# Optimization experiments

Measured on AMD Instinct MI355X. Metric: run time of the kernel, lower is better.

The kernel has to match this reference:

```python
import jax, jax.numpy as jnp
import numpy as np

B, NQ, NK = 4, 2048, 2048
D_MODEL, H, DK, DV, M = 512, 8, 64, 64, 40


def setup_inputs() -> dict:
    key = jax.random.key(0)
    ks = jax.random.split(key, 12)
    s = 0.02  # param init scale (stand-in for xavier)
    return {
        "queries": jax.random.normal(ks[0], (B, NQ, D_MODEL), jnp.float32),
        "keys": jax.random.normal(ks[1], (B, NK, D_MODEL), jnp.float32),
        "values": jax.random.normal(ks[2], (B, NK, D_MODEL), jnp.float32),
        "attention_weights": jax.random.uniform(ks[3], (B, H, NQ, NK), jnp.float32),
        "attention_mask": jax.random.randint(ks[4], (B, H, NQ, NK), 0, 2) == 1,
        "Wq": jax.random.normal(ks[5], (D_MODEL, H * DK), jnp.float32) * s,
        "bq": jnp.zeros((H * DK,), jnp.float32),
        "Wk": jax.random.normal(ks[6], (D_MODEL, H * DK), jnp.float32) * s,
        "bk": jnp.zeros((H * DK,), jnp.float32),
        "Wv": jax.random.normal(ks[7], (D_MODEL, H * DV), jnp.float32) * s,
        "bv": jnp.zeros((H * DV,), jnp.float32),
        "Wo": jax.random.normal(ks[8], (H * DV, D_MODEL), jnp.float32) * s,
        "bo": jnp.zeros((D_MODEL,), jnp.float32),
        "m_k": jax.random.normal(ks[9], (1, M, H * DK), jnp.float32) * s,
        "m_v": jax.random.normal(ks[10], (1, M, H * DV), jnp.float32) * s,
    }


def reference(queries, keys, values, attention_weights, attention_mask,
              Wq, bq, Wk, bk, Wv, bv, Wo, bo, m_k, m_v):
    b, nq, _ = queries.shape
    nk = keys.shape[1]
    # learned memory slots, scaled and broadcast over batch
    mk = jnp.sqrt(jnp.float32(DK)) * jnp.broadcast_to(m_k, (b, M, H * DK))
    mv = jnp.sqrt(jnp.float32(M)) * jnp.broadcast_to(m_v, (b, M, H * DV))
    q = (queries @ Wq + bq).reshape(b, nq, H, DK).transpose(0, 2, 1, 3)      # (b,h,nq,dk)
    k = jnp.concatenate([keys @ Wk + bk, mk], axis=1)
    k = k.reshape(b, nk + M, H, DK).transpose(0, 2, 3, 1)                     # (b,h,dk,nk+m)
    v = jnp.concatenate([values @ Wv + bv, mv], axis=1)
    v = v.reshape(b, nk + M, H, DV).transpose(0, 2, 1, 3)                     # (b,h,nk+m,dv)
    att = jnp.matmul(q, k) / jnp.sqrt(jnp.float32(DK))                        # (b,h,nq,nk+m)
    att_x = att[..., :nk] * attention_weights
    att_x = jnp.where(attention_mask, -jnp.inf, att_x)
    att = jnp.concatenate([att_x, att[..., nk:]], axis=-1)
    att = jax.nn.softmax(att, axis=-1)
    out = jnp.matmul(att, v).transpose(0, 2, 1, 3).reshape(b, nq, H * DV)
    return out @ Wo + bo
```

## Files before the change

kernel.cpp:

```cpp
#include <hip/hip_runtime.h>
#include <hip/hip_bf16.h>
#include <cstdint>
#include <cstddef>

typedef __bf16 bf16_t;
typedef __bf16 bf16x8 __attribute__((ext_vector_type(8)));
typedef __bf16 bf16x4 __attribute__((ext_vector_type(4)));
typedef float  f32x4  __attribute__((ext_vector_type(4)));

#define B_    4
#define NQ_   2048
#define NK_   2048
#define H_    8
#define MSL_  40
#define NKP_  2112
#define SCL2  0.18033688011112042f

#define GLOAD_LDS16(GP, LP)                                                        \
    __builtin_amdgcn_global_load_lds(                                              \
        (const __attribute__((address_space(1))) unsigned int*)(GP),               \
        (__attribute__((address_space(3))) unsigned int*)(LP), 16, 0, 0)

__global__ __launch_bounds__(256) void setup_fused(
    const float* __restrict__ Wq, const float* __restrict__ Wk,
    const float* __restrict__ Wv, const float* __restrict__ Wo,
    bf16_t* __restrict__ WqT, bf16_t* __restrict__ WkT,
    bf16_t* __restrict__ WvT, bf16_t* __restrict__ WoT,
    const float* __restrict__ m_k, const float* __restrict__ m_v,
    bf16_t* __restrict__ Kbf, bf16_t* __restrict__ Vt,
    const unsigned int* __restrict__ maskw, int* __restrict__ flag)
{
    __shared__ float t[32][33];
    __shared__ int found;
    const int blk = blockIdx.x;
    const int tid = threadIdx.x;

    if (blk < 1024) {
        const int bz = blk >> 8, by = (blk >> 4) & 15, bx = blk & 15;
        const float* src; bf16_t* dst;
        switch (bz) {
            case 0:  src = Wq; dst = WqT; break;
            case 1:  src = Wk; dst = WkT; break;
            case 2:  src = Wv; dst = WvT; break;
            default: src = Wo; dst = WoT; break;
        }
        const int tx = tid & 31, ty = tid >> 5;
        const int x  = bx * 32 + tx;
        const int y0 = by * 32 + ty;
#pragma unroll
        for (int i = 0; i < 32; i += 8)
            t[ty + i][tx] = src[(size_t)(y0 + i) * 512 + x];
        __syncthreads();
        const int ox  = by * 32 + tx;
        const int oy0 = bx * 32 + ty;
#pragma unroll
        for (int i = 0; i < 32; i += 8)
            dst[(size_t)(oy0 + i) * 512 + ox] = (bf16_t)t[tx][ty + i];
    } else if (blk < 2048) {
        int tt = (blk - 1024) * 256 + tid;
        if (tt < 4 * 64 * 512) {
            int c  = tt & 511;
            int mi = (tt >> 9) & 63;
            int b  = tt >> 15;
            float v = (mi < MSL_) ? 8.0f * m_k[mi * 512 + c] : 0.0f;
            Kbf[((size_t)b * NKP_ + NK_ + mi) * 512 + c] = (bf16_t)v;
        } else {
            int t2 = tt - 4 * 64 * 512;
            int mi = t2 & 63;
            int dv = (t2 >> 6) & 63;
            int h  = (t2 >> 12) & 7;
            int b  = t2 >> 15;
            float v = (mi < MSL_) ? 6.324555320336759f * m_v[mi * 512 + h * 64 + dv] : 0.0f;
            Vt[(((size_t)b * H_ + h) * 64 + dv) * NKP_ + NK_ + mi] = (bf16_t)v;
        }
    } else {
        if (tid == 0) found = 0;
        __syncthreads();
        unsigned int acc = 0;
        for (int i = tid; i < 65536; i += 256)
            acc |= (maskw[i] & 0xFFFFFF00u);
        if (acc) found = 1;
        __syncthreads();
        if (tid == 0) *flag = found;
    }
}

template<bool AF32>
__device__ __forceinline__ void gemm_core(
    bf16_t (*As)[128][72], bf16_t (*Bs)[128][72],
    const void* __restrict__ Av, const bf16_t* __restrict__ BT,
    const float* __restrict__ bias, void* __restrict__ dstv,
    int dstBS, int epi, float scale)
{
    const int tid = threadIdx.x;
    const int w = tid >> 6, l = tid & 63, lg = l >> 4, lr = l & 15;
    const int wr = w >> 1, wc = w & 1;
    const int blockM = blockIdx.x * 128, blockN = blockIdx.y * 128;

    f32x4 acc[4][4];
    const f32x4 zv = {0.f, 0.f, 0.f, 0.f};
#pragma unroll
    for (int i = 0; i < 4; i++)
#pragma unroll
        for (int j = 0; j < 4; j++) acc[i][j] = zv;

    const int ar = tid >> 1;
    const int ac = (tid & 1) * 32;

    float4 ra[8];
    uint4  ra16[4];
    uint4  rb[4];

#define GLOADT(K0) do {                                                           \
    if constexpr (AF32) {                                                         \
        const float* arow_ = (const float*)Av + (size_t)(blockM + ar) * 512 + (K0) + ac; \
        _Pragma("unroll") for (int i_ = 0; i_ < 8; i_++)                          \
            ra[i_] = ((const float4*)arow_)[i_];                                  \
    } else {                                                                      \
        const bf16_t* arow_ = (const bf16_t*)Av + (size_t)(blockM + ar) * 512 + (K0) + ac; \
        _Pragma("unroll") for (int i_ = 0; i_ < 4; i_++)                          \
            ra16[i_] = ((const uint4*)arow_)[i_];                                 \
    }                                                                             \
    const bf16_t* brow_ = BT + (size_t)(blockN + ar) * 512 + (K0) + ac;           \
    _Pragma("unroll") for (int i_ = 0; i_ < 4; i_++)                              \
        rb[i_] = ((const uint4*)brow_)[i_];                                       \
} while (0)

#define LDSWRITE(BUF) do {                                                        \
    if constexpr (AF32) {                                                         \
        _Pragma("unroll") for (int i_ = 0; i_ < 8; i_++) {                        \
            float4 v_ = ra[i_];                                                   \
            bf16x4 pk_ = {(bf16_t)v_.x, (bf16_t)v_.y, (bf16_t)v_.z, (bf16_t)v_.w}; \
            *(bf16x4*)&As[BUF][ar][ac + i_ * 4] = pk_;                            \
        }                                                                         \
    } else {                                                                      \
        _Pragma("unroll") for (int i_ = 0; i_ < 4; i_++)                          \
            *(uint4*)&As[BUF][ar][ac + i_ * 8] = ra16[i_];                        \
    }                                                                             \
    _Pragma("unroll") for (int i_ = 0; i_ < 4; i_++)                              \
        *(uint4*)&Bs[BUF][ar][ac + i_ * 8] = rb[i_];                              \
} while (0)

    GLOADT(0);
    LDSWRITE(0);

    for (int kk = 0; kk < 8; kk++) {
        __syncthreads();
        if (kk < 7) GLOADT((kk + 1) * 64);
        const int cb = kk & 1;
#pragma unroll
        for (int ks = 0; ks < 2; ks++) {
            bf16x8 af[4], bfr[4];
#pragma unroll
            for (int mi = 0; mi < 4; mi++)
                af[mi] = *(const bf16x8*)&As[cb][wr * 64 + mi * 16 + lr][ks * 32 + lg * 8];
#pragma unroll
            for (int ni = 0; ni < 4; ni++)
                bfr[ni] = *(const bf16x8*)&Bs[cb][wc * 64 + ni * 16 + lr][ks * 32 + lg * 8];
#pragma unroll
            for (int mi = 0; mi < 4; mi++)
#pragma unroll
                for (int ni = 0; ni < 4; ni++)
                    acc[mi][ni] = __builtin_amdgcn_mfma_f32_16x16x32_bf16(af[mi], bfr[ni], acc[mi][ni], 0, 0, 0);
        }
        if (kk < 7) LDSWRITE(cb ^ 1);
    }

#undef GLOADT
#undef LDSWRITE

    const int colbase = blockN + wc * 64;
    float bias_v[4];
#pragma unroll
    for (int ni = 0; ni < 4; ni++) bias_v[ni] = bias[colbase + ni * 16 + lr];

#pragma unroll
    for (int mi = 0; mi < 4; mi++) {
        const int r0 = blockM + wr * 64 + mi * 16 + lg * 4;
#pragma unroll
        for (int ni = 0; ni < 4; ni++) {
            const int c = colbase + ni * 16 + lr;
            f32x4 v = acc[mi][ni];
            if (epi == 2) {
                float* dst = (float*)dstv;
#pragma unroll
                for (int j = 0; j < 4; j++)
                    dst[(size_t)(r0 + j) * 512 + c] = (v[j] + bias_v[ni]) * scale;
            } else if (epi == 0) {
                bf16_t* dst = (bf16_t*)dstv;
#pragma unroll
                for (int j = 0; j < 4; j++) {
                    int rr = r0 + j;
                    int bb = rr >> 11, nn = rr & 2047;
                    dst[((size_t)bb * dstBS + nn) * 512 + c] = (bf16_t)((v[j] + bias_v[ni]) * scale);
                }
            } else {
                bf16_t* dst = (bf16_t*)dstv;
                int bb = r0 >> 11, n0 = r0 & 2047;
                int hh = c >> 6, dv = c & 63;
                bf16x4 pk;
#pragma unroll
                for (int j = 0; j < 4; j++) pk[j] = (bf16_t)((v[j] + bias_v[ni]) * scale);
                *(bf16x4*)(dst + (((size_t)bb * H_ + hh) * 64 + dv) * NKP_ + n0) = pk;
            }
        }
    }
}

__global__ __launch_bounds__(256) void gemm_qkv(
    const float* __restrict__ q, const float* __restrict__ k, const float* __restrict__ v,
    const bf16_t* __restrict__ WqT, const bf16_t* __restrict__ WkT, const bf16_t* __restrict__ WvT,
    const float* __restrict__ bq, const float* __restrict__ bk, const float* __restrict__ bv,
    bf16_t* __restrict__ Qbf, bf16_t* __restrict__ Kbf, bf16_t* __restrict__ Vt)
{
    __shared__ bf16_t As[2][128][72];
    __shared__ bf16_t Bs[2][128][72];
    const void* Av; const bf16_t* BT; const float* bias; void* dst;
    int dstBS, epi; float scale = 1.0f;
    switch (blockIdx.z) {
        case 0:  Av = q; BT = WqT; bias = bq; dst = Qbf; dstBS = 2048; epi = 0; scale = SCL2; break;
        case 1:  Av = k; BT = WkT; bias = bk; dst = Kbf; dstBS = NKP_; epi = 0; break;
        default: Av = v; BT = WvT; bias = bv; dst = Vt;  dstBS = 0;    epi = 1; break;
    }
    gemm_core<true>(As, Bs, Av, BT, bias, dst, dstBS, epi, scale);
}

__global__ __launch_bounds__(256) void gemm_fin(
    const bf16_t* __restrict__ Obuf, const bf16_t* __restrict__ WoT,
    const float* __restrict__ bo, float* __restrict__ out)
{
    __shared__ bf16_t As[2][128][72];
    __shared__ bf16_t Bs[2][128][72];
    gemm_core<false>(As, Bs, Obuf, WoT, bo, out, 0, 2, 1.0f);
}

template<bool BYTEM>
__global__ __launch_bounds__(512) void attn_fused(
    const bf16_t* __restrict__ Qbf, const bf16_t* __restrict__ Kbf,
    const bf16_t* __restrict__ Vt, const float* __restrict__ attw,
    const void* __restrict__ maskv, const int* __restrict__ mflag,
    bf16_t* __restrict__ Obuf)
{
    if ((*mflag != 0) != BYTEM) return;

    __shared__ bf16_t Ks[4][64][64];
    __shared__ bf16_t Vs[4][64][64];
    __shared__ bf16_t Pl[8][1024];

    const int tid = threadIdx.x;
    const int wv = tid >> 6, l = tid & 63, lg = l >> 4, lr = l & 15;
    const int qt = blockIdx.x, h = blockIdx.y, b = blockIdx.z;
    const int q0w = qt * 128 + wv * 16;
    bf16_t* Pw = &Pl[wv][0];

    const size_t bh = (size_t)(b * H_ + h);
    const float* wbase = attw + bh * (size_t)NQ_ * NK_;
    const unsigned char* mb8 = (const unsigned char*)maskv + bh * (size_t)NQ_ * NK_;
    const int* mb32 = (const int*)maskv + bh * (size_t)NQ_ * NK_;
    const char* kbase8 = (const char*)(Kbf + (size_t)b * NKP_ * 512 + h * 64);
    const char* vbase8 = (const char*)(Vt + bh * 64 * (size_t)NKP_);

    bf16x8 qf0 = *(const bf16x8*)&Qbf[((size_t)b * NQ_ + q0w + lr) * 512 + h * 64 + lg * 8];
    bf16x8 qf1 = *(const bf16x8*)&Qbf[((size_t)b * NQ_ + q0w + lr) * 512 + h * 64 + 32 + lg * 8];

    const f32x4 zv = {0.f, 0.f, 0.f, 0.f};
    f32x4 oacc[4];
#pragma unroll
    for (int i = 0; i < 4; i++) oacc[i] = zv;
    float lsum = 0.f;
    f32x4 sA[4];

    f32x4 wA[4], wB[4];
    unsigned mA[4], mB[4];
    unsigned miA[16], miB[16];

    const int srow = l >> 3;
    const int scsw = ((l & 7) ^ (srow & 7)) * 16;

#define STAGE(BUF, KCB) do {                                                      \
    const int r_ = wv * 8 + srow;                                                 \
    GLOAD_LDS16(kbase8 + (size_t)((KCB) + r_) * 1024 + scsw,                      \
                (char*)&Ks[BUF][0][0] + wv * 1024);                               \
    GLOAD_LDS16(vbase8 + (size_t)r_ * 4224 + (size_t)(KCB) * 2 + scsw,            \
                (char*)&Vs[BUF][0][0] + wv * 1024);                               \
} while (0)

#define PREFETCH(KT, WB_, MB_, MIB_) do {                                         \
    const float* wp_ = wbase + (size_t)(q0w + lr) * NK_ + (KT) * 64 + lg * 4;     \
    _Pragma("unroll") for (int n_ = 0; n_ < 4; n_++)                              \
        WB_[n_] = *(const f32x4*)(wp_ + n_ * 16);                                 \
    if constexpr (BYTEM) {                                                        \
        const unsigned char* mp_ = mb8 + (size_t)(q0w + lr) * NK_ + (KT) * 64 + lg * 4; \
        _Pragma("unroll") for (int n_ = 0; n_ < 4; n_++)                          \
            MB_[n_] = *(const unsigned*)(mp_ + n_ * 16);                          \
    } else {                                                                      \
        const int* mp_ = mb32 + (size_t)(q0w + lr) * NK_ + (KT) * 64 + lg * 4;    \
        _Pragma("unroll") for (int n_ = 0; n_ < 4; n_++) {                        \
            uint4 t_ = *(const uint4*)(mp_ + n_ * 16);                            \
            MIB_[n_ * 4 + 0] = t_.x; MIB_[n_ * 4 + 1] = t_.y;                     \
            MIB_[n_ * 4 + 2] = t_.z; MIB_[n_ * 4 + 3] = t_.w; }                   \
    }                                                                             \
} while (0)

#define QKT_LDS(BC) do {                                                          \
    const int sw_ = (lg ^ (lr & 7)) * 8;                                          \
    _Pragma("unroll") for (int n_ = 0; n_ < 4; n_++) {                            \
        const int kr_ = n_ * 16 + lr;                                             \
        f32x4 a_ = zv;                                                            \
        a_ = __builtin_amdgcn_mfma_f32_16x16x32_bf16(*(const bf16x8*)&Ks[BC][kr_][sw_], qf0, a_, 0, 0, 0); \
        a_ = __builtin_amdgcn_mfma_f32_16x16x32_bf16(*(const bf16x8*)&Ks[BC][kr_][sw_ ^ 32], qf1, a_, 0, 0, 0); \
        sA[n_] = a_;                                                              \
    }                                                                             \
} while (0)

#define APPLY(WB_, MB_, MIB_) do {                                                \
    _Pragma("unroll") for (int n_ = 0; n_ < 4; n_++)                              \
    _Pragma("unroll") for (int j_ = 0; j_ < 4; j_++) {                            \
        bool mk_;                                                                 \
        if constexpr (BYTEM) mk_ = ((MB_[n_] >> (8 * j_)) & 0xffu) != 0;          \
        else                 mk_ = (MIB_[n_ * 4 + j_] != 0);                      \
        sA[n_][j_] = mk_ ? -1e30f : sA[n_][j_] * WB_[n_][j_];                     \
    }                                                                             \
} while (0)

#define SMPV(BC) do {                                                             \
    _Pragma("unroll") for (int n_ = 0; n_ < 4; n_++)                              \
    _Pragma("unroll") for (int j_ = 0; j_ < 4; j_++) {                            \
        float p_ = exp2f(sA[n_][j_]);                                             \
        sA[n_][j_] = p_; lsum += p_;                                              \
    }                                                                             \
    _Pragma("unroll") for (int n_ = 0; n_ < 4; n_++) {                            \
        int c_ = n_ * 2 + (lg >> 1);                                              \
        int qp_ = (lr + 4 * c_) & 15;                                             \
        bf16x4 pk_ = {(bf16_t)sA[n_][0], (bf16_t)sA[n_][1],                       \
                      (bf16_t)sA[n_][2], (bf16_t)sA[n_][3]};                      \
        *(bf16x4*)&Pw[c_ * 128 + qp_ * 8 + (lg & 1) * 4] = pk_;                   \
    }                                                                             \
    bf16x8 pf0_ = *(const bf16x8*)&Pw[lg * 128 + ((lr + 4 * lg) & 15) * 8];       \
    bf16x8 pf1_ = *(const bf16x8*)&Pw[(4 + lg) * 128 + ((lr + 4 * (4 + lg)) & 15) * 8]; \
    const int vsw_ = (lg ^ (lr & 7)) * 8;                                         \
    _Pragma("unroll") for (int n2_ = 0; n2_ < 4; n2_++) {                         \
        const int vr_ = n2_ * 16 + lr;                                            \
        oacc[n2_] = __builtin_amdgcn_mfma_f32_16x16x32_bf16(*(const bf16x8*)&Vs[BC][vr_][vsw_], pf0_, oacc[n2_], 0, 0, 0); \
        oacc[n2_] = __builtin_amdgcn_mfma_f32_16x16x32_bf16(*(const bf16x8*)&Vs[BC][vr_][vsw_ ^ 32], pf1_, oacc[n2_], 0, 0, 0); \
    }                                                                             \
} while (0)

#define SUBB(T, BC, W_, M_, MI_) do {                                            \
    QKT_LDS(BC);                                                                  \
    APPLY(W_, M_, MI_);                                                           \
    if ((T) < 30) PREFETCH((T) + 2, W_, M_, MI_);                                 \
    SMPV(BC);                                                                     \
} while (0)

#define PERIOD(T, B0, B1, S0, S1) do {                                            \
    if ((T) + 2 < 32) STAGE(S0, ((T) + 2) * 64);                                  \
    if ((T) + 3 < 32) STAGE(S1, ((T) + 3) * 64);                                  \
    SUBB((T),     B0, wA, mA, miA);                                               \
    SUBB((T) + 1, B1, wB, mB, miB);                                               \
    __syncthreads();                                                              \
} while (0)

    STAGE(0, 2048);
    STAGE(1, 0);
    STAGE(2, 64);
    PREFETCH(0, wA, mA, miA);
    __syncthreads();

    {
        QKT_LDS(0);
#pragma unroll
        for (int n_ = 0; n_ < 4; n_++)
#pragma unroll
            for (int j_ = 0; j_ < 4; j_++) {
                int kloc = n_ * 16 + lg * 4 + j_;
                sA[n_][j_] = (kloc >= MSL_) ? -1e30f : sA[n_][j_];
            }
        PREFETCH(1, wB, mB, miB);
        SMPV(0);
        __syncthreads();
    }

    for (int t = 0; t < 28; t += 4) {
        PERIOD(t,     1, 2, 3, 0);
        PERIOD(t + 2, 3, 0, 1, 2);
    }
    PERIOD(28, 1, 2, 3, 0);
    SUBB(30, 3, wA, mA, miA);
    SUBB(31, 0, wB, mB, miB);

    float ts = lsum;
    ts += __shfl_xor(ts, 16);
    ts += __shfl_xor(ts, 32);
    float invl = 1.0f / ts;
#pragma unroll
    for (int n2 = 0; n2 < 4; n2++) {
        bf16x4 ov = {(bf16_t)(oacc[n2][0] * invl), (bf16_t)(oacc[n2][1] * invl),
                     (bf16_t)(oacc[n2][2] * invl), (bf16_t)(oacc[n2][3] * invl)};
        *(bf16x4*)&Obuf[((size_t)b * NQ_ + q0w + lr) * 512 + h * 64 + n2 * 16 + lg * 4] = ov;
    }

#undef STAGE
#undef PREFETCH
#undef QKT_LDS
#undef APPLY
#undef SMPV
#undef SUBB
#undef PERIOD
}

extern "C" void kernel_launch(void* const* d_in, const int* in_sizes, int n_in,
                              void* d_out, int out_size, void* d_ws, size_t ws_size,
                              hipStream_t stream)
{
    const float* queries = (const float*)d_in[0];
    const float* keys    = (const float*)d_in[1];
    const float* values  = (const float*)d_in[2];
    const float* attw    = (const float*)d_in[3];
    const void*  maskv   = d_in[4];
    const float* Wq = (const float*)d_in[5];
    const float* bq = (const float*)d_in[6];
    const float* Wk = (const float*)d_in[7];
    const float* bk = (const float*)d_in[8];
    const float* Wv = (const float*)d_in[9];
    const float* bv = (const float*)d_in[10];
    const float* Wo = (const float*)d_in[11];
    const float* bo = (const float*)d_in[12];
    const float* m_k = (const float*)d_in[13];
    const float* m_v = (const float*)d_in[14];

    char* ws = (char*)d_ws;
    bf16_t* WqT  = (bf16_t*)(ws + 0);
    bf16_t* WkT  = (bf16_t*)(ws + 524288);
    bf16_t* WvT  = (bf16_t*)(ws + 1048576);
    bf16_t* WoT  = (bf16_t*)(ws + 1572864);
    bf16_t* Qbf  = (bf16_t*)(ws + 2097152);
    bf16_t* Kbf  = (bf16_t*)(ws + 10485760);
    bf16_t* Vt   = (bf16_t*)(ws + 19136512);
    bf16_t* Obuf = (bf16_t*)(ws + 27787264);
    int*    mflag = (int*)(ws + 36175872);

    setup_fused<<<2049, 256, 0, stream>>>(
        Wq, Wk, Wv, Wo, WqT, WkT, WvT, WoT,
        m_k, m_v, Kbf, Vt, (const unsigned int*)maskv, mflag);

    gemm_qkv<<<dim3(64, 4, 3), 256, 0, stream>>>(
        queries, keys, values, WqT, WkT, WvT, bq, bk, bv, Qbf, Kbf, Vt);

    attn_fused<true><<<dim3(16, H_, B_), 512, 0, stream>>>(Qbf, Kbf, Vt, attw, maskv, mflag, Obuf);
    attn_fused<false><<<dim3(16, H_, B_), 512, 0, stream>>>(Qbf, Kbf, Vt, attw, maskv, mflag, Obuf);

    gemm_fin<<<dim3(64, 4), 256, 0, stream>>>(Obuf, WoT, bo, (float*)d_out);
    (void)in_sizes; (void)n_in; (void)out_size; (void)ws_size;
}
```

Baseline: 357.6 us.

## Deepen attention pipeline to four tiles of K/V and weight/mask prefetch

Doubles the K/V LDS ring from 4 to 8 buffers and keeps four register sets of attention-weight and mask data in flight instead of two. Prefetch distance grows from 2 to 4 tiles, and each period now processes four key tiles per barrier. The aim is to hide more global-memory latency on the large weight and mask streams and to cut barriers. In exchange LDS use rises to about 144KB per block and VGPR pressure grows, which likely drops occupancy to one block per CU and may cause spills.

```diff
diff --git a/kernel.cpp b/kernel.cpp
--- a/kernel.cpp
+++ b/kernel.cpp
@@ -243,8 +243,8 @@
 {
     if ((*mflag != 0) != BYTEM) return;
 
-    __shared__ bf16_t Ks[4][64][64];
-    __shared__ bf16_t Vs[4][64][64];
+    __shared__ bf16_t Ks[8][64][64];
+    __shared__ bf16_t Vs[8][64][64];
     __shared__ bf16_t Pl[8][1024];
 
     const int tid = threadIdx.x;
@@ -270,9 +270,9 @@
     float lsum = 0.f;
     f32x4 sA[4];
 
-    f32x4 wA[4], wB[4];
-    unsigned mA[4], mB[4];
-    unsigned miA[16], miB[16];
+    f32x4 wA[4], wB[4], wC[4], wD[4];
+    unsigned mA[4], mB[4], mC[4], mD[4];
+    unsigned miA[16], miB[16], miC[16], miD[16];
 
     const int srow = l >> 3;
     const int scsw = ((l & 7) ^ (srow & 7)) * 16;
@@ -349,25 +349,37 @@
 #define SUBB(T, BC, W_, M_, MI_) do {                                            \
     QKT_LDS(BC);                                                                  \
     APPLY(W_, M_, MI_);                                                           \
-    if ((T) < 30) PREFETCH((T) + 2, W_, M_, MI_);                                 \
+    if ((T) < 28) PREFETCH((T) + 4, W_, M_, MI_);                                 \
     SMPV(BC);                                                                     \
 } while (0)
 
-#define PERIOD(T, B0, B1, S0, S1) do {                                            \
-    if ((T) + 2 < 32) STAGE(S0, ((T) + 2) * 64);                                  \
-    if ((T) + 3 < 32) STAGE(S1, ((T) + 3) * 64);                                  \
-    SUBB((T),     B0, wA, mA, miA);                                               \
-    SUBB((T) + 1, B1, wB, mB, miB);                                               \
+#define PERIOD(T, B0, B1, B2, B3, S0, S1, S2, S3) do {                            \
+    if ((T) + 4 < 32) STAGE(S0, ((T) + 4) * 64);                                  \
+    if ((T) + 5 < 32) STAGE(S1, ((T) + 5) * 64);                                  \
+    if ((T) + 6 < 32) STAGE(S2, ((T) + 6) * 64);                                  \
+    if ((T) + 7 < 32) STAGE(S3, ((T) + 7) * 64);                                  \
+    SUBB((T),     B0, wD, mD, miD);                                               \
+    SUBB((T) + 1, B1, wA, mA, miA);                                               \
+    SUBB((T) + 2, B2, wB, mB, miB);                                               \
+    SUBB((T) + 3, B3, wC, mC, miC);                                               \
     __syncthreads();                                                              \
 } while (0)
 
     STAGE(0, 2048);
     STAGE(1, 0);
     STAGE(2, 64);
+    STAGE(3, 128);
     PREFETCH(0, wA, mA, miA);
+    PREFETCH(1, wB, mB, miB);
+    PREFETCH(2, wC, mC, miC);
+    PREFETCH(3, wD, mD, miD);
     __syncthreads();
 
     {
+        STAGE(4, 3 * 64);
+        STAGE(5, 4 * 64);
+        STAGE(6, 5 * 64);
+        STAGE(7, 6 * 64);
         QKT_LDS(0);
 #pragma unroll
         for (int n_ = 0; n_ < 4; n_++)
@@ -376,18 +388,21 @@
                 int kloc = n_ * 16 + lg * 4 + j_;
                 sA[n_][j_] = (kloc >= MSL_) ? -1e30f : sA[n_][j_];
             }
-        PREFETCH(1, wB, mB, miB);
         SMPV(0);
+        SUBB(0, 1, wA, mA, miA);
+        SUBB(1, 2, wB, mB, miB);
+        SUBB(2, 3, wC, mC, miC);
         __syncthreads();
     }
 
-    for (int t = 0; t < 28; t += 4) {
-        PERIOD(t,     1, 2, 3, 0);
-        PERIOD(t + 2, 3, 0, 1, 2);
-    }
-    PERIOD(28, 1, 2, 3, 0);
-    SUBB(30, 3, wA, mA, miA);
-    SUBB(31, 0, wB, mB, miB);
+    PERIOD(3,  4, 5, 6, 7,  0, 1, 2, 3);
+    PERIOD(7,  0, 1, 2, 3,  4, 5, 6, 7);
+    PERIOD(11, 4, 5, 6, 7,  0, 1, 2, 3);
+    PERIOD(15, 0, 1, 2, 3,  4, 5, 6, 7);
+    PERIOD(19, 4, 5, 6, 7,  0, 1, 2, 3);
+    PERIOD(23, 0, 1, 2, 3,  4, 5, 6, 7);
+    PERIOD(27, 4, 5, 6, 7,  0, 1, 2, 3);
+    SUBB(31, 0, wD, mD, miD);
 
     float ts = lsum;
     ts += __shfl_xor(ts, 16);
```

Measured after the change: 389.3 us. 8.9% more time.
